# Optimization experiments

Hardware: AMD Instinct MI355X
Metric: run time of the kernel (lower is better)

## Reference

```python
import jax, jax.numpy as jnp
import numpy as np

N_CARD, N_TX, N_MER = 100_000, 1_000_000, 10_000
E = 1_000_000
H = 128


def setup_inputs() -> dict:
    key = jax.random.key(0)
    ks = iter(jax.random.split(key, 32))
    nrm = lambda shape, s=1.0: jax.random.normal(next(ks), shape, jnp.float32) * s
    W = 0.05  # weight scale for numerical sanity across two relu layers
    inp = {
        "x_card": nrm((N_CARD, 32)),
        "x_tx": nrm((N_TX, 64)),
        "x_mer": nrm((N_MER, 32)),
        # layer-1 SAGEConv params per edge type: lin_l (src->H, w/ bias), lin_r (dst->H)
        "l1_pays_wl": nrm((32, H), W), "l1_pays_bl": nrm((H,), W), "l1_pays_wr": nrm((64, H), W),
        "l1_recv_wl": nrm((32, H), W), "l1_recv_bl": nrm((H,), W), "l1_recv_wr": nrm((64, H), W),
        "l1_rpays_wl": nrm((64, H), W), "l1_rpays_bl": nrm((H,), W), "l1_rpays_wr": nrm((32, H), W),
        "l1_rrecv_wl": nrm((64, H), W), "l1_rrecv_bl": nrm((H,), W), "l1_rrecv_wr": nrm((32, H), W),
        # layer-2: all relations are H->H; stacked in order [pays, receives, rev_pays, rev_receives]
        "w2l": nrm((4, H, H), W), "b2": nrm((4, H), W), "w2r": nrm((4, H, H), W),
        # final lazy Linear(-1, out_channels=1) -> (H, 1)
        "wf": nrm((H, 1), W), "bf": nrm((1,), W),
        "pays_src": jax.random.randint(next(ks), (E,), 0, N_CARD, jnp.int32),
        "pays_dst": jnp.arange(E, dtype=jnp.int32),
        "recv_src": jax.random.randint(next(ks), (E,), 0, N_MER, jnp.int32),
        "recv_dst": jnp.arange(E, dtype=jnp.int32),
    }
    return inp


def _sage(x_src, x_dst, src, dst, wl, bl, wr, n_dst):
    """PyG SAGEConv(aggr='mean'): lin_l(mean_j x_j) + lin_r(x_root)."""
    msg = x_src[src]  # [E, d_src] gather
    s = jax.ops.segment_sum(msg, dst, num_segments=n_dst)
    cnt = jax.ops.segment_sum(jnp.ones((src.shape[0], 1), msg.dtype), dst, num_segments=n_dst)
    mean = s / jnp.maximum(cnt, 1.0)
    return mean @ wl + bl + x_dst @ wr


def reference(x_card, x_tx, x_mer,
              l1_pays_wl, l1_pays_bl, l1_pays_wr,
              l1_recv_wl, l1_recv_bl, l1_recv_wr,
              l1_rpays_wl, l1_rpays_bl, l1_rpays_wr,
              l1_rrecv_wl, l1_rrecv_bl, l1_rrecv_wr,
              w2l, b2, w2r, wf, bf,
              pays_src, pays_dst, recv_src, recv_dst):
    # ---- layer 1 (HeteroConv aggr='sum' over relations sharing a dst type) ----
    tx = (_sage(x_card, x_tx, pays_src, pays_dst, l1_pays_wl, l1_pays_bl, l1_pays_wr, N_TX)
          + _sage(x_mer, x_tx, recv_src, recv_dst, l1_recv_wl, l1_recv_bl, l1_recv_wr, N_TX))
    # rev_pays / rev_receives are the transposed edge lists
    card = _sage(x_tx, x_card, pays_dst, pays_src, l1_rpays_wl, l1_rpays_bl, l1_rpays_wr, N_CARD)
    mer = _sage(x_tx, x_mer, recv_dst, recv_src, l1_rrecv_wl, l1_rrecv_bl, l1_rrecv_wr, N_MER)
    tx, card, mer = jax.nn.relu(tx), jax.nn.relu(card), jax.nn.relu(mer)
    # ---- layer 2 (only transaction output feeds the head; card/mer layer-2 outputs unused) ----
    tx2 = (_sage(card, tx, pays_src, pays_dst, w2l[0], b2[0], w2r[0], N_TX)
           + _sage(mer, tx, recv_src, recv_dst, w2l[1], b2[1], w2r[1], N_TX))
    tx2 = jax.nn.relu(tx2)
    return tx2 @ wf + bf  # [N_TX, 1]
```

## Files before the change

kernel.cpp:

```cpp
#include <hip/hip_runtime.h>
#include <hip/hip_bf16.h>
#include <stdint.h>

#define NCARD 100000
#define NTX   1000000
#define NMER  10000
#define NE    1000000
#define CAPC  48
#define CAPM  192
#define NCB   3125
#define NMB   313


typedef __attribute__((ext_vector_type(8))) short bf16x8;
typedef __attribute__((ext_vector_type(4))) float f32x4;

__device__ inline unsigned short f2bf(float f) {
  union { float f; uint32_t u; } v; v.f = f;
  uint32_t r = v.u + 0x7FFF + ((v.u >> 16) & 1);
  return (unsigned short)(r >> 16);
}
__device__ inline float bf2f(unsigned short u) {
  union { uint32_t u; float f; } v; v.u = ((uint32_t)u) << 16;
  return v.f;
}
__device__ inline uint32_t addpack2(uint32_t a, uint32_t b) {
  float lo = bf2f((unsigned short)(a & 0xffff)) + bf2f((unsigned short)(b & 0xffff));
  float hi = bf2f((unsigned short)(a >> 16))   + bf2f((unsigned short)(b >> 16));
  return (uint32_t)f2bf(lo) | ((uint32_t)f2bf(hi) << 16);
}

#define OFF_WR1T  0u
#define OFF_W2RT  4096u
#define OFF_B1    12288u
#define OFF_B2    12416u
#define OFF_CW1   12544u
#define OFF_CW2   18688u
#define OFF_CW3   26880u
#define OFF_MW1   28928u
#define OFF_MW2   35072u
#define OFF_MW3   43264u
#define OFF_CQ    45312u
#define OFF_MQ    12845312u
#define OFF_CCNT  14125312u
#define OFF_MCNT  14225312u
#define OFF_CBUK  14235312u
#define OFF_MBUK  19035312u
#define OFF_XB    20955312u
#define WS_END    52955312u

__global__ __launch_bounds__(256) void k_prep_all(
    const float* __restrict__ pays_wr, const float* __restrict__ recv_wr,
    const float* __restrict__ w2r, const float* __restrict__ pays_bl,
    const float* __restrict__ recv_bl, const float* __restrict__ b2,
    unsigned short* __restrict__ wr1t, unsigned short* __restrict__ w2rt,
    float* __restrict__ b1sum, float* __restrict__ b2sum,
    const float* __restrict__ c_wl64, const float* __restrict__ c_wr32,
    const float* __restrict__ c_w2, const float* __restrict__ c_wg,
    unsigned short* __restrict__ cw1, unsigned short* __restrict__ cw2,
    unsigned short* __restrict__ cw3,
    const float* __restrict__ m_wl64, const float* __restrict__ m_wr32,
    const float* __restrict__ m_w2, const float* __restrict__ m_wg,
    unsigned short* __restrict__ mw1, unsigned short* __restrict__ mw2,
    unsigned short* __restrict__ mw3)
{
  const int grp = blockIdx.x >> 6;
  const int i = (blockIdx.x & 63) * 256 + threadIdx.x;
  if (grp == 0) {
    if (i < 8192) {
      int n = i >> 6, k = i & 63;
      wr1t[i] = f2bf(pays_wr[k * 128 + n] + recv_wr[k * 128 + n]);
    }
    if (i < 16384) {
      int n = i >> 7, k = i & 127;
      w2rt[i] = f2bf(w2r[k * 128 + n] + w2r[16384 + k * 128 + n]);
    }
    if (i < 128) {
      b1sum[i] = pays_bl[i] + recv_bl[i];
      b2sum[i] = b2[i] + b2[128 + i];
    }
  } else {
    const float* wl64 = (grp == 1) ? c_wl64 : m_wl64;
    const float* wr32 = (grp == 1) ? c_wr32 : m_wr32;
    const float* w2   = (grp == 1) ? c_w2   : m_w2;
    const float* wg   = (grp == 1) ? c_wg   : m_wg;
    unsigned short* w1t = (grp == 1) ? cw1 : mw1;
    unsigned short* w2t = (grp == 1) ? cw2 : mw2;
    unsigned short* w3t = (grp == 1) ? cw3 : mw3;
    if (i < 12288) {
      int n = i / 96, k = i % 96;
      float v = (k < 64) ? wl64[k * 128 + n] : wr32[(k - 64) * 128 + n];
      w1t[i] = f2bf(v);
    }
    if (i < 16384) { int n = i >> 7, k = i & 127; w2t[i] = f2bf(w2[k * 128 + n]); }
    if (i < 4096)  { int n = i >> 5, k = i & 31;  w3t[i] = f2bf(wg[k * 128 + n]); }
  }
}

__global__ __launch_bounds__(256) void k_convert_build(
    const float* __restrict__ x, unsigned short* __restrict__ xb,
    const int* __restrict__ ps, const int* __restrict__ rs,
    int* __restrict__ ccnt, int* __restrict__ mcnt,
    int* __restrict__ cbuk, int* __restrict__ mbuk)
{
  int64_t i = (int64_t)blockIdx.x * 256 + threadIdx.x;
  if (i < 16000000) {
    float4 v = ((const float4*)x)[i];
    unsigned short p[4] = { f2bf(v.x), f2bf(v.y), f2bf(v.z), f2bf(v.w) };
    *(uint2*)&xb[i * 4] = *(const uint2*)p;
  }
  if (i < NE) {
    int e = (int)i;
    int c = ps[e];
    int pos = atomicAdd(ccnt + c, 1);
    if (pos < CAPC) cbuk[c * CAPC + pos] = e;
    int m = rs[e];
    int pm = atomicAdd(mcnt + m, 1);
    if (pm < CAPM) mbuk[m * CAPM + pm] = e;
  }
}

__global__ __launch_bounds__(256) void k_node_both(
    const int* __restrict__ ccnt, const int* __restrict__ cbuk,
    const int* __restrict__ mcnt, const int* __restrict__ mbuk,
    const unsigned short* __restrict__ xb,
    const float* __restrict__ x_card, const float* __restrict__ x_mer,
    const unsigned short* __restrict__ cw1, const unsigned short* __restrict__ cw2,
    const unsigned short* __restrict__ cw3, const float* __restrict__ cbl,
    const unsigned short* __restrict__ mw1, const unsigned short* __restrict__ mw2,
    const unsigned short* __restrict__ mw3, const float* __restrict__ mbl,
    const float* __restrict__ b1sum, const float* __restrict__ b2sum,
    unsigned short* __restrict__ cq, unsigned short* __restrict__ mq)
{
  const bool iscard = blockIdx.x < NCB;
  const int* cnt = iscard ? ccnt : mcnt;
  const int* buk = iscard ? cbuk : mbuk;
  const int cap  = iscard ? CAPC : CAPM;
  const int R    = iscard ? NCARD : NMER;
  const float* x_node = iscard ? x_card : x_mer;
  const unsigned short* w1t = iscard ? cw1 : mw1;
  const unsigned short* w2t = iscard ? cw2 : mw2;
  const unsigned short* w3t = iscard ? cw3 : mw3;
  const float* bl = iscard ? cbl : mbl;
  unsigned short* q = iscard ? cq : mq;
  const int n0 = (iscard ? blockIdx.x : blockIdx.x - NCB) * 32;

  __shared__ unsigned short ms[32 * 64];
  __shared__ unsigned short xs2[32 * 32];
  __shared__ unsigned short ts[32 * 128];
  __shared__ float bll[128], ba1[128], ba2[128];
  const int tid = threadIdx.x;
  const int wv = tid >> 6, l = tid & 63;
  const int lr = l & 15, lk = l >> 4;

  bf16x8 f1[2][3], f2w[2][4], f3[2];
#pragma unroll
  for (int c = 0; c < 2; ++c) {
    const int n = wv * 32 + c * 16 + lr;
#pragma unroll
    for (int k = 0; k < 3; ++k)
      f1[c][k] = *(const bf16x8*)(w1t + n * 96 + k * 32 + lk * 8);
#pragma unroll
    for (int k = 0; k < 4; ++k)
      f2w[c][k] = *(const bf16x8*)(w2t + n * 128 + k * 32 + lk * 8);
    f3[c] = *(const bf16x8*)(w3t + n * 32 + lk * 8);
  }
  if (tid < 128) {
    bll[tid] = bl[tid];
    ba1[tid] = iscard ? b1sum[tid] : 0.f;
    ba2[tid] = iscard ? b2sum[tid] : 0.f;
  }

  const int half = l >> 5, c32 = l & 31;
  for (int rr = wv; rr < 32; rr += 4) {
    const int node = n0 + rr;
    int deg = 0;
    if (node < R) deg = cnt[node];
    const int64_t base = (int64_t)node * cap;
    float a0 = 0.f, a1 = 0.f;
    int p = half;
    for (; p + 6 < deg; p += 8) {
      int e0 = buk[base + p],     e1 = buk[base + p + 2];
      int e2 = buk[base + p + 4], e3 = buk[base + p + 6];
      uint32_t v0 = *(const uint32_t*)&xb[(int64_t)e0 * 64 + c32 * 2];
      uint32_t v1 = *(const uint32_t*)&xb[(int64_t)e1 * 64 + c32 * 2];
      uint32_t v2 = *(const uint32_t*)&xb[(int64_t)e2 * 64 + c32 * 2];
      uint32_t v3 = *(const uint32_t*)&xb[(int64_t)e3 * 64 + c32 * 2];
      a0 += bf2f((unsigned short)(v0 & 0xffff)) + bf2f((unsigned short)(v1 & 0xffff))
          + bf2f((unsigned short)(v2 & 0xffff)) + bf2f((unsigned short)(v3 & 0xffff));
      a1 += bf2f((unsigned short)(v0 >> 16)) + bf2f((unsigned short)(v1 >> 16))
          + bf2f((unsigned short)(v2 >> 16)) + bf2f((unsigned short)(v3 >> 16));
    }
    for (; p < deg; p += 2) {
      int e = buk[base + p];
      uint32_t v = *(const uint32_t*)&xb[(int64_t)e * 64 + c32 * 2];
      a0 += bf2f((unsigned short)(v & 0xffff));
      a1 += bf2f((unsigned short)(v >> 16));
    }
    a0 += __shfl_xor(a0, 32, 64);
    a1 += __shfl_xor(a1, 32, 64);
    if (half == 0) {
      float inv = 1.f / fmaxf((float)deg, 1.f);
      unsigned short pr[2] = { f2bf(a0 * inv), f2bf(a1 * inv) };
      int li = (rr * 64 + c32 * 2) ^ ((rr & 7) << 3);
      *(uint32_t*)&ms[li] = *(const uint32_t*)pr;
    }
  }
#pragma unroll
  for (int q4 = 0; q4 < 4; ++q4) {
    int id = q4 * 256 + tid;
    int r = id >> 5, c = id & 31;
    float v = (n0 + r < R) ? x_node[(int64_t)(n0 + r) * 32 + c] : 0.f;
    xs2[(r * 32 + c) ^ ((r & 3) << 3)] = f2bf(v);
  }
  __syncthreads();

#pragma unroll
  for (int rt = 0; rt < 2; ++rt) {
    const int arow = rt * 16 + lr;
    const int sw = (arow & 7) << 3, sw2 = (arow & 3) << 3;
    bf16x8 a0 = *(const bf16x8*)&ms[(arow * 64 + 0  + lk * 8) ^ sw];
    bf16x8 a1 = *(const bf16x8*)&ms[(arow * 64 + 32 + lk * 8) ^ sw];
    bf16x8 ax = *(const bf16x8*)&xs2[(arow * 32 + lk * 8) ^ sw2];
    f32x4 acc0 = {0.f,0.f,0.f,0.f}, acc1 = {0.f,0.f,0.f,0.f};
    acc0 = __builtin_amdgcn_mfma_f32_16x16x32_bf16(a0, f1[0][0], acc0, 0, 0, 0);
    acc0 = __builtin_amdgcn_mfma_f32_16x16x32_bf16(a1, f1[0][1], acc0, 0, 0, 0);
    acc0 = __builtin_amdgcn_mfma_f32_16x16x32_bf16(ax, f1[0][2], acc0, 0, 0, 0);
    acc1 = __builtin_amdgcn_mfma_f32_16x16x32_bf16(a0, f1[1][0], acc1, 0, 0, 0);
    acc1 = __builtin_amdgcn_mfma_f32_16x16x32_bf16(a1, f1[1][1], acc1, 0, 0, 0);
    acc1 = __builtin_amdgcn_mfma_f32_16x16x32_bf16(ax, f1[1][2], acc1, 0, 0, 0);
#pragma unroll
    for (int c = 0; c < 2; ++c) {
      const int col = wv * 32 + c * 16 + lr;
#pragma unroll
      for (int i = 0; i < 4; ++i) {
        const int r = rt * 16 + lk * 4 + i;
        float v = (c ? acc1[i] : acc0[i]) + bll[col];
        ts[(r * 128 + col) ^ ((r & 7) << 3)] = f2bf(fmaxf(v, 0.f));
      }
    }
  }
  __syncthreads();

#pragma unroll
  for (int rt = 0; rt < 2; ++rt) {
    const int arow = rt * 16 + lr;
    const int sw = (arow & 7) << 3, sw2 = (arow & 3) << 3;
    f32x4 b0 = {0.f,0.f,0.f,0.f}, b1a = {0.f,0.f,0.f,0.f};
#pragma unroll
    for (int kk = 0; kk < 4; ++kk) {
      bf16x8 a = *(const bf16x8*)&ts[(arow * 128 + kk * 32 + lk * 8) ^ sw];
      b0  = __builtin_amdgcn_mfma_f32_16x16x32_bf16(a, f2w[0][kk], b0, 0, 0, 0);
      b1a = __builtin_amdgcn_mfma_f32_16x16x32_bf16(a, f2w[1][kk], b1a, 0, 0, 0);
    }
    bf16x8 ax = *(const bf16x8*)&xs2[(arow * 32 + lk * 8) ^ sw2];
    f32x4 g0 = {0.f,0.f,0.f,0.f}, g1a = {0.f,0.f,0.f,0.f};
    g0  = __builtin_amdgcn_mfma_f32_16x16x32_bf16(ax, f3[0], g0, 0, 0, 0);
    g1a = __builtin_amdgcn_mfma_f32_16x16x32_bf16(ax, f3[1], g1a, 0, 0, 0);
#pragma unroll
    for (int c = 0; c < 2; ++c) {
#pragma unroll
      for (int i = 0; i < 4; ++i) {
        const int node = n0 + rt * 16 + lk * 4 + i;
        const int col = wv * 32 + c * 16 + lr;
        if (node < R) {
          q[node * 256 + col]       = f2bf((c ? g1a[i] : g0[i]) + ba1[col]);
          q[node * 256 + 128 + col] = f2bf((c ? b1a[i] : b0[i]) + ba2[col]);
        }
      }
    }
  }
}

#define TXR 32
__global__ __launch_bounds__(256) void k_fused_tx_mfma(
    const unsigned short* __restrict__ xb,
    const int* __restrict__ ps, const int* __restrict__ rs,
    const unsigned short* __restrict__ cq, const unsigned short* __restrict__ mq,
    const unsigned short* __restrict__ wr1t, const unsigned short* __restrict__ w2rt,
    const float* __restrict__ wf, const float* __restrict__ bfp,
    float* __restrict__ out)
{
  __shared__ unsigned short xs[TXR * 64];
  __shared__ unsigned short ts[TXR * 128];
  __shared__ unsigned short g1[TXR * 128];
  __shared__ unsigned short g2[TXR * 128];
  __shared__ float partial[4][TXR];
  __shared__ float wfl[128];

  const int tid = threadIdx.x;
  const int wv = tid >> 6;
  const int l  = tid & 63;
  const int lr = l & 15;
  const int lk = l >> 4;

  bf16x8 w1f[2][2], w2f[2][4];
#pragma unroll
  for (int c = 0; c < 2; ++c) {
    const int n = (wv * 2 + c) * 16 + lr;
#pragma unroll
    for (int kk = 0; kk < 2; ++kk)
      w1f[c][kk] = *(const bf16x8*)(wr1t + n * 64 + kk * 32 + lk * 8);
#pragma unroll
    for (int kk = 0; kk < 4; ++kk)
      w2f[c][kk] = *(const bf16x8*)(w2rt + n * 128 + kk * 32 + lk * 8);
  }
  if (tid < 128) wfl[tid] = wf[tid];
  const float bfv = bfp[0];

  const uint32_t* cqd = (const uint32_t*)cq;
  const uint32_t* mqd = (const uint32_t*)mq;

  for (int64_t row0 = (int64_t)blockIdx.x * TXR; row0 < NTX;
       row0 += (int64_t)gridDim.x * TXR) {
    __syncthreads();
    {
      const int r = tid >> 3, seg = tid & 7;
      uint4 v = *(const uint4*)&xb[(row0 + r) * 64 + seg * 8];
      *(uint4*)&xs[(r * 64 + seg * 8) ^ ((r & 7) << 3)] = v;
    }
#pragma unroll
    for (int p = 0; p < 8; ++p) {
      const int r = p * 4 + wv;
      const int64_t c = ps[row0 + r];
      const int64_t m = rs[row0 + r];
      const int dst = r * 64 + (l ^ (p << 3));
      uint32_t a1 = cqd[c * 128 + l],      v1 = mqd[m * 128 + l];
      ((uint32_t*)g1)[dst] = addpack2(a1, v1);
      uint32_t a2 = cqd[c * 128 + 64 + l], v2 = mqd[m * 128 + 64 + l];
      ((uint32_t*)g2)[dst] = addpack2(a2, v2);
    }
    __syncthreads();

#pragma unroll
    for (int rt = 0; rt < 2; ++rt) {
      const int arow = rt * 16 + lr;
      const int sw = (arow & 7) << 3;
      bf16x8 a0  = *(const bf16x8*)&xs[(arow * 64 + 0  + lk * 8) ^ sw];
      bf16x8 a1v = *(const bf16x8*)&xs[(arow * 64 + 32 + lk * 8) ^ sw];
      f32x4 acc0 = {0.f,0.f,0.f,0.f}, acc1 = {0.f,0.f,0.f,0.f};
      acc0 = __builtin_amdgcn_mfma_f32_16x16x32_bf16(a0,  w1f[0][0], acc0, 0, 0, 0);
      acc0 = __builtin_amdgcn_mfma_f32_16x16x32_bf16(a1v, w1f[0][1], acc0, 0, 0, 0);
      acc1 = __builtin_amdgcn_mfma_f32_16x16x32_bf16(a0,  w1f[1][0], acc1, 0, 0, 0);
      acc1 = __builtin_amdgcn_mfma_f32_16x16x32_bf16(a1v, w1f[1][1], acc1, 0, 0, 0);
      const int gx = (rt * 4 + lk) << 3;
#pragma unroll
      for (int c = 0; c < 2; ++c) {
        const int col = wv * 32 + c * 16 + lr;
        const int gofs = (((col >> 1) ^ gx) << 1) + (col & 1);
        const f32x4 acc = c ? acc1 : acc0;
#pragma unroll
        for (int i = 0; i < 4; ++i) {
          const int r = rt * 16 + lk * 4 + i;
          float v = acc[i] + bf2f(g1[r * 128 + gofs]);
          ts[(r * 128 + col) ^ ((r & 7) << 3)] = f2bf(fmaxf(v, 0.f));
        }
      }
    }
    __syncthreads();

#pragma unroll
    for (int rt = 0; rt < 2; ++rt) {
      const int arow = rt * 16 + lr;
      const int sw = (arow & 7) << 3;
      f32x4 acc0 = {0.f,0.f,0.f,0.f}, acc1 = {0.f,0.f,0.f,0.f};
#pragma unroll
      for (int kk = 0; kk < 4; ++kk) {
        bf16x8 a = *(const bf16x8*)&ts[(arow * 128 + kk * 32 + lk * 8) ^ sw];
        acc0 = __builtin_amdgcn_mfma_f32_16x16x32_bf16(a, w2f[0][kk], acc0, 0, 0, 0);
        acc1 = __builtin_amdgcn_mfma_f32_16x16x32_bf16(a, w2f[1][kk], acc1, 0, 0, 0);
      }
      const int gx = (rt * 4 + lk) << 3;
#pragma unroll
      for (int i = 0; i < 4; ++i) {
        const int r = rt * 16 + lk * 4 + i;
        float sum = 0.f;
#pragma unroll
        for (int c = 0; c < 2; ++c) {
          const int col = wv * 32 + c * 16 + lr;
          const int gofs = (((col >> 1) ^ gx) << 1) + (col & 1);
          float y = (c ? acc1[i] : acc0[i]) + bf2f(g2[r * 128 + gofs]);
          sum = fmaf(fmaxf(y, 0.f), wfl[col], sum);
        }
#pragma unroll
        for (int off = 1; off < 16; off <<= 1) sum += __shfl_xor(sum, off, 64);
        if (lr == 0) partial[wv][r] = sum;
      }
    }
    __syncthreads();
    if (tid < TXR)
      out[row0 + tid] = partial[0][tid] + partial[1][tid] + partial[2][tid]
                      + partial[3][tid] + bfv;
  }
}

extern "C" void kernel_launch(void* const* d_in, const int* in_sizes, int n_in,
                              void* d_out, int out_size, void* d_ws, size_t ws_size,
                              hipStream_t stream) {
  const float* x_card = (const float*)d_in[0];
  const float* x_tx   = (const float*)d_in[1];
  const float* x_mer  = (const float*)d_in[2];
  const float* l1_pays_wl = (const float*)d_in[3];
  const float* l1_pays_bl = (const float*)d_in[4];
  const float* l1_pays_wr = (const float*)d_in[5];
  const float* l1_recv_wl = (const float*)d_in[6];
  const float* l1_recv_bl = (const float*)d_in[7];
  const float* l1_recv_wr = (const float*)d_in[8];
  const float* l1_rpays_wl = (const float*)d_in[9];
  const float* l1_rpays_bl = (const float*)d_in[10];
  const float* l1_rpays_wr = (const float*)d_in[11];
  const float* l1_rrecv_wl = (const float*)d_in[12];
  const float* l1_rrecv_bl = (const float*)d_in[13];
  const float* l1_rrecv_wr = (const float*)d_in[14];
  const float* w2l = (const float*)d_in[15];
  const float* b2  = (const float*)d_in[16];
  const float* w2r = (const float*)d_in[17];
  const float* wf  = (const float*)d_in[18];
  const float* bf  = (const float*)d_in[19];
  const int* pays_src = (const int*)d_in[20];
  const int* recv_src = (const int*)d_in[22];

  float* ws = (float*)d_ws;
  unsigned short* wr1t = (unsigned short*)(ws + OFF_WR1T);
  unsigned short* w2rt = (unsigned short*)(ws + OFF_W2RT);
  float* b1sum = ws + OFF_B1;
  float* b2sum = ws + OFF_B2;
  unsigned short* cw1 = (unsigned short*)(ws + OFF_CW1);
  unsigned short* cw2 = (unsigned short*)(ws + OFF_CW2);
  unsigned short* cw3 = (unsigned short*)(ws + OFF_CW3);
  unsigned short* mw1 = (unsigned short*)(ws + OFF_MW1);
  unsigned short* mw2 = (unsigned short*)(ws + OFF_MW2);
  unsigned short* mw3 = (unsigned short*)(ws + OFF_MW3);
  unsigned short* cq  = (unsigned short*)(ws + OFF_CQ);
  unsigned short* mq  = (unsigned short*)(ws + OFF_MQ);
  int* ccnt = (int*)(ws + OFF_CCNT);
  int* mcnt = (int*)(ws + OFF_MCNT);
  int* cbuk = (int*)(ws + OFF_CBUK);
  int* mbuk = (int*)(ws + OFF_MBUK);
  unsigned short* xb = (unsigned short*)(ws + OFF_XB);

  hipMemsetAsync((char*)d_ws + (size_t)OFF_CCNT * 4, 0,
                 (size_t)(OFF_CBUK - OFF_CCNT) * 4, stream);

  k_prep_all<<<192, 256, 0, stream>>>(
      l1_pays_wr, l1_recv_wr, w2r, l1_pays_bl, l1_recv_bl, b2,
      wr1t, w2rt, b1sum, b2sum,
      l1_rpays_wl, l1_rpays_wr, w2l, l1_pays_wl, cw1, cw2, cw3,
      l1_rrecv_wl, l1_rrecv_wr, w2l + 16384, l1_recv_wl, mw1, mw2, mw3);

  k_convert_build<<<62500, 256, 0, stream>>>(x_tx, xb, pays_src, recv_src,
                                             ccnt, mcnt, cbuk, mbuk);

  k_node_both<<<NCB + NMB, 256, 0, stream>>>(
      ccnt, cbuk, mcnt, mbuk, xb, x_card, x_mer,
      cw1, cw2, cw3, l1_rpays_bl,
      mw1, mw2, mw3, l1_rrecv_bl,
      b1sum, b2sum, cq, mq);

  k_fused_tx_mfma<<<2048, 256, 0, stream>>>(xb, pays_src, recv_src, cq, mq,
                                            wr1t, w2rt, wf, bf, (float*)d_out);
}
```

Before: 683.0 us.

## Compute card layer-1 gather term in tx kernel instead of materializing per-card

The card node kernel no longer writes a 256-wide per-card row containing the precomputed x_card@W_pays_l term. Instead x_card is converted to bf16 alongside x_tx, and the fused tx kernel gathers each transaction's 32-wide card feature row and applies an extra MFMA against that weight. Bias sums move to the merchant rows so the total stays the same. This shrinks the card intermediate from 256 to 128 columns, cutting gather traffic per transaction, at the cost of an extra small gather and two extra MFMAs per tile.

```diff
diff --git a/kernel.cpp b/kernel.cpp
--- a/kernel.cpp
+++ b/kernel.cpp
@@ -41,13 +41,14 @@
 #define OFF_MW2   35072u
 #define OFF_MW3   43264u
 #define OFF_CQ    45312u
-#define OFF_MQ    12845312u
-#define OFF_CCNT  14125312u
-#define OFF_MCNT  14225312u
-#define OFF_CBUK  14235312u
-#define OFF_MBUK  19035312u
-#define OFF_XB    20955312u
-#define WS_END    52955312u
+#define OFF_MQ    6445312u
+#define OFF_XCB   7725312u
+#define OFF_CCNT  9325312u
+#define OFF_MCNT  9425312u
+#define OFF_CBUK  9435312u
+#define OFF_MBUK  14235312u
+#define OFF_XB    16155312u
+#define WS_END    48155312u
 
 __global__ __launch_bounds__(256) void k_prep_all(
     const float* __restrict__ pays_wr, const float* __restrict__ recv_wr,
@@ -99,6 +100,7 @@
 
 __global__ __launch_bounds__(256) void k_convert_build(
     const float* __restrict__ x, unsigned short* __restrict__ xb,
+    const float* __restrict__ xc, unsigned short* __restrict__ xcb,
     const int* __restrict__ ps, const int* __restrict__ rs,
     int* __restrict__ ccnt, int* __restrict__ mcnt,
     int* __restrict__ cbuk, int* __restrict__ mbuk)
@@ -108,6 +110,11 @@
     float4 v = ((const float4*)x)[i];
     unsigned short p[4] = { f2bf(v.x), f2bf(v.y), f2bf(v.z), f2bf(v.w) };
     *(uint2*)&xb[i * 4] = *(const uint2*)p;
+  }
+  if (i < 800000) {
+    float4 v = ((const float4*)xc)[i];
+    unsigned short p[4] = { f2bf(v.x), f2bf(v.y), f2bf(v.z), f2bf(v.w) };
+    *(uint2*)&xcb[i * 4] = *(const uint2*)p;
   }
   if (i < NE) {
     int e = (int)i;
@@ -142,7 +149,6 @@
   const unsigned short* w2t = iscard ? cw2 : mw2;
   const unsigned short* w3t = iscard ? cw3 : mw3;
   const float* bl = iscard ? cbl : mbl;
-  unsigned short* q = iscard ? cq : mq;
   const int n0 = (iscard ? blockIdx.x : blockIdx.x - NCB) * 32;
 
   __shared__ unsigned short ms[32 * 64];
@@ -167,8 +173,8 @@
   }
   if (tid < 128) {
     bll[tid] = bl[tid];
-    ba1[tid] = iscard ? b1sum[tid] : 0.f;
-    ba2[tid] = iscard ? b2sum[tid] : 0.f;
+    ba1[tid] = iscard ? 0.f : b1sum[tid];
+    ba2[tid] = iscard ? 0.f : b2sum[tid];
   }
 
   const int half = l >> 5, c32 = l & 31;
@@ -253,19 +259,31 @@
       b0  = __builtin_amdgcn_mfma_f32_16x16x32_bf16(a, f2w[0][kk], b0, 0, 0, 0);
       b1a = __builtin_amdgcn_mfma_f32_16x16x32_bf16(a, f2w[1][kk], b1a, 0, 0, 0);
     }
-    bf16x8 ax = *(const bf16x8*)&xs2[(arow * 32 + lk * 8) ^ sw2];
-    f32x4 g0 = {0.f,0.f,0.f,0.f}, g1a = {0.f,0.f,0.f,0.f};
-    g0  = __builtin_amdgcn_mfma_f32_16x16x32_bf16(ax, f3[0], g0, 0, 0, 0);
-    g1a = __builtin_amdgcn_mfma_f32_16x16x32_bf16(ax, f3[1], g1a, 0, 0, 0);
-#pragma unroll
-    for (int c = 0; c < 2; ++c) {
-#pragma unroll
-      for (int i = 0; i < 4; ++i) {
-        const int node = n0 + rt * 16 + lk * 4 + i;
-        const int col = wv * 32 + c * 16 + lr;
-        if (node < R) {
-          q[node * 256 + col]       = f2bf((c ? g1a[i] : g0[i]) + ba1[col]);
-          q[node * 256 + 128 + col] = f2bf((c ? b1a[i] : b0[i]) + ba2[col]);
+    if (iscard) {
+#pragma unroll
+      for (int c = 0; c < 2; ++c) {
+#pragma unroll
+        for (int i = 0; i < 4; ++i) {
+          const int node = n0 + rt * 16 + lk * 4 + i;
+          const int col = wv * 32 + c * 16 + lr;
+          if (node < R) cq[node * 128 + col] = f2bf(c ? b1a[i] : b0[i]);
+        }
+      }
+    } else {
+      bf16x8 ax = *(const bf16x8*)&xs2[(arow * 32 + lk * 8) ^ sw2];
+      f32x4 g0 = {0.f,0.f,0.f,0.f}, g1a = {0.f,0.f,0.f,0.f};
+      g0  = __builtin_amdgcn_mfma_f32_16x16x32_bf16(ax, f3[0], g0, 0, 0, 0);
+      g1a = __builtin_amdgcn_mfma_f32_16x16x32_bf16(ax, f3[1], g1a, 0, 0, 0);
+#pragma unroll
+      for (int c = 0; c < 2; ++c) {
+#pragma unroll
+        for (int i = 0; i < 4; ++i) {
+          const int node = n0 + rt * 16 + lk * 4 + i;
+          const int col = wv * 32 + c * 16 + lr;
+          if (node < R) {
+            mq[node * 256 + col]       = f2bf((c ? g1a[i] : g0[i]) + ba1[col]);
+            mq[node * 256 + 128 + col] = f2bf((c ? b1a[i] : b0[i]) + ba2[col]);
+          }
         }
       }
     }
@@ -275,13 +293,16 @@
 #define TXR 32
 __global__ __launch_bounds__(256) void k_fused_tx_mfma(
     const unsigned short* __restrict__ xb,
+    const unsigned short* __restrict__ xcb,
     const int* __restrict__ ps, const int* __restrict__ rs,
     const unsigned short* __restrict__ cq, const unsigned short* __restrict__ mq,
     const unsigned short* __restrict__ wr1t, const unsigned short* __restrict__ w2rt,
+    const unsigned short* __restrict__ wgt,
     const float* __restrict__ wf, const float* __restrict__ bfp,
     float* __restrict__ out)
 {
   __shared__ unsigned short xs[TXR * 64];
+  __shared__ unsigned short xcs[TXR * 32];
   __shared__ unsigned short ts[TXR * 128];
   __shared__ unsigned short g1[TXR * 128];
   __shared__ unsigned short g2[TXR * 128];
@@ -294,7 +315,7 @@
   const int lr = l & 15;
   const int lk = l >> 4;
 
-  bf16x8 w1f[2][2], w2f[2][4];
+  bf16x8 w1f[2][2], w2f[2][4], wgf[2];
 #pragma unroll
   for (int c = 0; c < 2; ++c) {
     const int n = (wv * 2 + c) * 16 + lr;
@@ -304,6 +325,7 @@
 #pragma unroll
     for (int kk = 0; kk < 4; ++kk)
       w2f[c][kk] = *(const bf16x8*)(w2rt + n * 128 + kk * 32 + lk * 8);
+    wgf[c] = *(const bf16x8*)(wgt + n * 32 + lk * 8);
   }
   if (tid < 128) wfl[tid] = wf[tid];
   const float bfv = bfp[0];
@@ -319,16 +341,20 @@
       uint4 v = *(const uint4*)&xb[(row0 + r) * 64 + seg * 8];
       *(uint4*)&xs[(r * 64 + seg * 8) ^ ((r & 7) << 3)] = v;
     }
+    if (tid < 128) {
+      const int r = tid >> 2, seg = tid & 3;
+      const int64_t c = ps[row0 + r];
+      uint4 v = *(const uint4*)&xcb[c * 32 + seg * 8];
+      *(uint4*)&xcs[(r * 32 + seg * 8) ^ ((r & 3) << 3)] = v;
+    }
 #pragma unroll
     for (int p = 0; p < 8; ++p) {
       const int r = p * 4 + wv;
       const int64_t c = ps[row0 + r];
       const int64_t m = rs[row0 + r];
       const int dst = r * 64 + (l ^ (p << 3));
-      uint32_t a1 = cqd[c * 128 + l],      v1 = mqd[m * 128 + l];
-      ((uint32_t*)g1)[dst] = addpack2(a1, v1);
-      uint32_t a2 = cqd[c * 128 + 64 + l], v2 = mqd[m * 128 + 64 + l];
-      ((uint32_t*)g2)[dst] = addpack2(a2, v2);
+      ((uint32_t*)g1)[dst] = mqd[m * 128 + l];
+      ((uint32_t*)g2)[dst] = addpack2(cqd[c * 64 + l], mqd[m * 128 + 64 + l]);
     }
     __syncthreads();
 
@@ -338,11 +364,14 @@
       const int sw = (arow & 7) << 3;
       bf16x8 a0  = *(const bf16x8*)&xs[(arow * 64 + 0  + lk * 8) ^ sw];
       bf16x8 a1v = *(const bf16x8*)&xs[(arow * 64 + 32 + lk * 8) ^ sw];
+      bf16x8 axc = *(const bf16x8*)&xcs[(arow * 32 + lk * 8) ^ ((arow & 3) << 3)];
       f32x4 acc0 = {0.f,0.f,0.f,0.f}, acc1 = {0.f,0.f,0.f,0.f};
       acc0 = __builtin_amdgcn_mfma_f32_16x16x32_bf16(a0,  w1f[0][0], acc0, 0, 0, 0);
       acc0 = __builtin_amdgcn_mfma_f32_16x16x32_bf16(a1v, w1f[0][1], acc0, 0, 0, 0);
+      acc0 = __builtin_amdgcn_mfma_f32_16x16x32_bf16(axc, wgf[0],    acc0, 0, 0, 0);
       acc1 = __builtin_amdgcn_mfma_f32_16x16x32_bf16(a0,  w1f[1][0], acc1, 0, 0, 0);
       acc1 = __builtin_amdgcn_mfma_f32_16x16x32_bf16(a1v, w1f[1][1], acc1, 0, 0, 0);
+      acc1 = __builtin_amdgcn_mfma_f32_16x16x32_bf16(axc, wgf[1],    acc1, 0, 0, 0);
       const int gx = (rt * 4 + lk) << 3;
 #pragma unroll
       for (int c = 0; c < 2; ++c) {
@@ -433,6 +462,7 @@
   unsigned short* mw3 = (unsigned short*)(ws + OFF_MW3);
   unsigned short* cq  = (unsigned short*)(ws + OFF_CQ);
   unsigned short* mq  = (unsigned short*)(ws + OFF_MQ);
+  unsigned short* xcb = (unsigned short*)(ws + OFF_XCB);
   int* ccnt = (int*)(ws + OFF_CCNT);
   int* mcnt = (int*)(ws + OFF_MCNT);
   int* cbuk = (int*)(ws + OFF_CBUK);
@@ -448,7 +478,8 @@
       l1_rpays_wl, l1_rpays_wr, w2l, l1_pays_wl, cw1, cw2, cw3,
       l1_rrecv_wl, l1_rrecv_wr, w2l + 16384, l1_recv_wl, mw1, mw2, mw3);
 
-  k_convert_build<<<62500, 256, 0, stream>>>(x_tx, xb, pays_src, recv_src,
+  k_convert_build<<<62500, 256, 0, stream>>>(x_tx, xb, x_card, xcb,
+                                             pays_src, recv_src,
                                              ccnt, mcnt, cbuk, mbuk);
 
   k_node_both<<<NCB + NMB, 256, 0, stream>>>(
@@ -457,6 +488,7 @@
       mw1, mw2, mw3, l1_rrecv_bl,
       b1sum, b2sum, cq, mq);
 
-  k_fused_tx_mfma<<<2048, 256, 0, stream>>>(xb, pays_src, recv_src, cq, mq,
-                                            wr1t, w2rt, wf, bf, (float*)d_out);
-}
+  k_fused_tx_mfma<<<2048, 256, 0, stream>>>(xb, xcb, pays_src, recv_src, cq, mq,
+                                            wr1t, w2rt, cw3, wf, bf,
+                                            (float*)d_out);
+}
```

New measurement: 707.5 us. 3.6% more time.

## Prefetch next tile's gathers into registers and widen aggregation unroll

Applied to the files above, without the earlier changes.

The persistent transaction-row loop now issues the global loads for the next tile (x rows and the card/merchant gathered rows) into registers before doing the MFMA work on the current tile. This overlaps gather latency with compute. The bucket aggregation loop also gets a 16-wide step with all index and value loads batched up front, to raise memory-level parallelism. Both changes add register pressure, which can reduce occupancy.

```diff
diff --git a/kernel.cpp b/kernel.cpp
--- a/kernel.cpp
+++ b/kernel.cpp
@@ -179,6 +179,20 @@
     const int64_t base = (int64_t)node * cap;
     float a0 = 0.f, a1 = 0.f;
     int p = half;
+    for (; p + 14 < deg; p += 16) {
+      int ei[8];
+      uint32_t vi[8];
+#pragma unroll
+      for (int u = 0; u < 8; ++u) ei[u] = buk[base + p + 2 * u];
+#pragma unroll
+      for (int u = 0; u < 8; ++u)
+        vi[u] = *(const uint32_t*)&xb[(int64_t)ei[u] * 64 + c32 * 2];
+#pragma unroll
+      for (int u = 0; u < 8; ++u) {
+        a0 += bf2f((unsigned short)(vi[u] & 0xffff));
+        a1 += bf2f((unsigned short)(vi[u] >> 16));
+      }
+    }
     for (; p + 6 < deg; p += 8) {
       int e0 = buk[base + p],     e1 = buk[base + p + 2];
       int e2 = buk[base + p + 4], e3 = buk[base + p + 6];
@@ -311,26 +325,49 @@
   const uint32_t* cqd = (const uint32_t*)cq;
   const uint32_t* mqd = (const uint32_t*)mq;
 
-  for (int64_t row0 = (int64_t)blockIdx.x * TXR; row0 < NTX;
-       row0 += (int64_t)gridDim.x * TXR) {
-    __syncthreads();
-    {
-      const int r = tid >> 3, seg = tid & 7;
-      uint4 v = *(const uint4*)&xb[(row0 + r) * 64 + seg * 8];
-      *(uint4*)&xs[(r * 64 + seg * 8) ^ ((r & 7) << 3)] = v;
-    }
+  const int r_x = tid >> 3, seg_x = tid & 7;
+  const int64_t stride = (int64_t)gridDim.x * TXR;
+  int64_t row0 = (int64_t)blockIdx.x * TXR;
+
+  uint4 xv;
+  uint32_t rc1[8], rm1[8], rc2[8], rm2[8];
+
+  if (row0 < NTX) {
+    xv = *(const uint4*)&xb[(row0 + r_x) * 64 + seg_x * 8];
 #pragma unroll
     for (int p = 0; p < 8; ++p) {
       const int r = p * 4 + wv;
       const int64_t c = ps[row0 + r];
       const int64_t m = rs[row0 + r];
+      rc1[p] = cqd[c * 128 + l];      rm1[p] = mqd[m * 128 + l];
+      rc2[p] = cqd[c * 128 + 64 + l]; rm2[p] = mqd[m * 128 + 64 + l];
+    }
+  }
+
+  for (; row0 < NTX; row0 += stride) {
+    __syncthreads();
+    *(uint4*)&xs[(r_x * 64 + seg_x * 8) ^ ((r_x & 7) << 3)] = xv;
+#pragma unroll
+    for (int p = 0; p < 8; ++p) {
+      const int r = p * 4 + wv;
       const int dst = r * 64 + (l ^ (p << 3));
-      uint32_t a1 = cqd[c * 128 + l],      v1 = mqd[m * 128 + l];
-      ((uint32_t*)g1)[dst] = addpack2(a1, v1);
-      uint32_t a2 = cqd[c * 128 + 64 + l], v2 = mqd[m * 128 + 64 + l];
-      ((uint32_t*)g2)[dst] = addpack2(a2, v2);
+      ((uint32_t*)g1)[dst] = addpack2(rc1[p], rm1[p]);
+      ((uint32_t*)g2)[dst] = addpack2(rc2[p], rm2[p]);
     }
     __syncthreads();
+
+    const int64_t nxt = row0 + stride;
+    if (nxt < NTX) {
+      xv = *(const uint4*)&xb[(nxt + r_x) * 64 + seg_x * 8];
+#pragma unroll
+      for (int p = 0; p < 8; ++p) {
+        const int r = p * 4 + wv;
+        const int64_t c = ps[nxt + r];
+        const int64_t m = rs[nxt + r];
+        rc1[p] = cqd[c * 128 + l];      rm1[p] = mqd[m * 128 + l];
+        rc2[p] = cqd[c * 128 + 64 + l]; rm2[p] = mqd[m * 128 + 64 + l];
+      }
+    }
 
 #pragma unroll
     for (int rt = 0; rt < 2; ++rt) {
```

Result: faster. 649.5 us (-4.9%).
